# Kernel optimization log

Hardware: AMD Instinct MI355X
Metric: run time of the kernel (lower is better)

Reference implementation:

```python
import jax, jax.numpy as jnp
import numpy as np

EPS = 1e-05
NEG = -1e9

def rotate_half(x):
    x1, x2 = jnp.split(x, 2, axis=-1)
    return jnp.concatenate([-x2, x1], axis=-1)

def rmsnorm(x, w):
    xf = x.astype(jnp.float32)
    n = xf * jax.lax.rsqrt(jnp.mean(xf * xf, axis=-1, keepdims=True) + EPS)
    return w * n.astype(x.dtype)

def setup_inputs() -> dict:
    key = jax.random.key(0)
    ks = jax.random.split(key, 12)
    B, S, H, NH, DH, FF = 1, 2048, 2048, 16, 128, 8192
    x = jax.random.normal(ks[0], (B, S, H), jnp.float32)
    # additive causal mask [1,1,S,S]
    causal = jnp.where(jnp.tril(jnp.ones((S, S), bool)), 0.0, NEG).astype(jnp.float32)
    attention_mask = causal[None, None]
    alibi = 0.1 * jax.random.normal(ks[1], (1, NH, S, S), jnp.float32)
    # rotary angles [S, DH]
    inv = 1.0 / (10000.0 ** (jnp.arange(0, DH, 2, dtype=jnp.float32) / DH))
    ang = jnp.arange(S, dtype=jnp.float32)[:, None] * inv[None, :]
    freqs = jnp.concatenate([ang, ang], axis=-1)  # [S, DH]
    sc = 1.0 / np.sqrt(H)
    wq = sc * jax.random.normal(ks[2], (H, H), jnp.float32)
    wk = sc * jax.random.normal(ks[3], (H, H), jnp.float32)
    wv = sc * jax.random.normal(ks[4], (H, H), jnp.float32)
    wo = sc * jax.random.normal(ks[5], (H, H), jnp.float32)
    w1 = sc * jax.random.normal(ks[6], (H, FF), jnp.float32)
    w3 = sc * jax.random.normal(ks[7], (H, FF), jnp.float32)
    w2 = (1.0 / np.sqrt(FF)) * jax.random.normal(ks[8], (FF, H), jnp.float32)
    attn_norm_w = jnp.ones((H,), jnp.float32)
    ffn_norm_w = jnp.ones((H,), jnp.float32)
    return dict(x=x, attention_mask=attention_mask, alibi=alibi, freqs=freqs,
                wq=wq, wk=wk, wv=wv, wo=wo, w1=w1, w2=w2, w3=w3,
                attn_norm_w=attn_norm_w, ffn_norm_w=ffn_norm_w)

def reference(x, attention_mask, alibi, freqs, wq, wk, wv, wo, w1, w2, w3,
              attn_norm_w, ffn_norm_w):
    B, S, H = x.shape
    NH = 16
    DH = H // NH
    nx = rmsnorm(x, attn_norm_w)
    # projections -> [B, NH, S, DH]
    def heads(y):
        return y.reshape(B, S, NH, DH).transpose(0, 2, 1, 3)
    q = heads(nx @ wq)
    k = heads(nx @ wk)
    v = heads(nx @ wv)
    cos, sin = jnp.cos(freqs), jnp.sin(freqs)  # [S, DH] broadcasts over B,NH
    q = q * cos + rotate_half(q) * sin
    k = k * cos + rotate_half(k) * sin
    scores = jnp.einsum('bhqd,bhkd->bhqk', q, k) / np.sqrt(DH)
    scores = scores + attention_mask + alibi
    attn = jax.nn.softmax(scores, axis=-1)
    out = jnp.einsum('bhqk,bhkd->bhqd', attn, v)
    out = out.transpose(0, 2, 1, 3).reshape(B, S, H)
    x = x + out @ wo
    nx = rmsnorm(x, ffn_norm_w)
    ff = (jax.nn.silu(nx @ w1) * (nx @ w3)) @ w2
    return x + ff
```

## Files before the change

### kernel.cpp

```cpp
#include <hip/hip_runtime.h>
#include <hip/hip_bf16.h>
#include <math.h>

typedef __bf16 bf16x8 __attribute__((ext_vector_type(8)));
typedef float  f32x4  __attribute__((ext_vector_type(4)));
typedef unsigned short u16x8 __attribute__((ext_vector_type(8)));
typedef unsigned short u16x4 __attribute__((ext_vector_type(4)));

#define DEV static __device__ __forceinline__

DEV void gload16(const void* g, void* l) {
  __builtin_amdgcn_global_load_lds((__attribute__((address_space(1))) void*)g,
                                   (__attribute__((address_space(3))) void*)l,
                                   16, 0, 0);
}

DEV float bf2f(unsigned short u) {
  unsigned v = ((unsigned)u) << 16;
  return __builtin_bit_cast(float, v);
}
DEV unsigned short f2bf(float f) {
  unsigned u = __builtin_bit_cast(unsigned, f);
  u = u + 0x7fffu + ((u >> 16) & 1u);
  return (unsigned short)(u >> 16);
}

__global__ __launch_bounds__(256) void rmsnorm_k(const float* __restrict__ x,
    const float* __restrict__ w, unsigned short* __restrict__ out, int H) {
  int row = blockIdx.x;
  const float4* xr = (const float4*)(x + (size_t)row * H);
  float4 a = xr[threadIdx.x * 2], b = xr[threadIdx.x * 2 + 1];
  float ss = a.x*a.x + a.y*a.y + a.z*a.z + a.w*a.w
           + b.x*b.x + b.y*b.y + b.z*b.z + b.w*b.w;
#pragma unroll
  for (int o = 32; o; o >>= 1) ss += __shfl_down(ss, o, 64);
  __shared__ float red[4];
  if ((threadIdx.x & 63) == 0) red[threadIdx.x >> 6] = ss;
  __syncthreads();
  float rs = rsqrtf((red[0] + red[1] + red[2] + red[3]) * (1.0f / 2048.0f) + 1e-5f);
  size_t base = (size_t)row * H + threadIdx.x * 8;
  const float* wv = w + threadIdx.x * 8;
  float vals[8] = {a.x, a.y, a.z, a.w, b.x, b.y, b.z, b.w};
  u16x8 o8;
#pragma unroll
  for (int i = 0; i < 8; ++i) o8[i] = f2bf(vals[i] * rs * wv[i]);
  *(u16x8*)(out + base) = o8;
}

__global__ __launch_bounds__(256) void reduce4rms_k(const float* __restrict__ part,
    const float* __restrict__ resid, const float* __restrict__ w,
    float* __restrict__ x2, unsigned short* __restrict__ nxo, int H, size_t mn) {
  const int row = blockIdx.x, t = threadIdx.x;
  size_t base = (size_t)row * H + t * 8;
  float v[8];
  {
    float4 a = ((const float4*)(resid + base))[0];
    float4 b = ((const float4*)(resid + base))[1];
    v[0]=a.x; v[1]=a.y; v[2]=a.z; v[3]=a.w; v[4]=b.x; v[5]=b.y; v[6]=b.z; v[7]=b.w;
  }
#pragma unroll
  for (int s = 0; s < 4; ++s) {
    const float4* p4 = (const float4*)(part + (size_t)s * mn + base);
    float4 pa = p4[0], pb = p4[1];
    v[0]+=pa.x; v[1]+=pa.y; v[2]+=pa.z; v[3]+=pa.w;
    v[4]+=pb.x; v[5]+=pb.y; v[6]+=pb.z; v[7]+=pb.w;
  }
  float ss = 0.f;
#pragma unroll
  for (int i = 0; i < 8; ++i) ss += v[i] * v[i];
  float4 o0 = {v[0],v[1],v[2],v[3]}, o1 = {v[4],v[5],v[6],v[7]};
  ((float4*)(x2 + base))[0] = o0;
  ((float4*)(x2 + base))[1] = o1;
#pragma unroll
  for (int o = 32; o; o >>= 1) ss += __shfl_down(ss, o, 64);
  __shared__ float red[4];
  if ((t & 63) == 0) red[t >> 6] = ss;
  __syncthreads();
  float rs = rsqrtf((red[0] + red[1] + red[2] + red[3]) * (1.0f / 2048.0f) + 1e-5f);
  const float* wv = w + t * 8;
  u16x8 o8;
#pragma unroll
  for (int i = 0; i < 8; ++i) o8[i] = f2bf(v[i] * rs * wv[i]);
  *(u16x8*)(nxo + base) = o8;
}

DEV void wtrans_body(const float* __restrict__ W, unsigned short* __restrict__ Wt,
                     int R, int C, int ilv, int bx, int by, int t,
                     unsigned short (*tile)[68]) {
  const int c0 = bx * 64, r0 = by * 64;
  const int lr = t >> 4, lc4 = (t & 15) * 4;
#pragma unroll
  for (int i = 0; i < 4; ++i) {
    float4 v = *(const float4*)&W[(size_t)(r0 + lr + i * 16) * C + c0 + lc4];
    u16x4 s4;
    s4[0] = f2bf(v.x); s4[1] = f2bf(v.y); s4[2] = f2bf(v.z); s4[3] = f2bf(v.w);
    *(u16x4*)&tile[lr + i * 16][lc4] = s4;
  }
  __syncthreads();
  const int oc = t >> 3, seg = (t & 7) * 8;
#pragma unroll
  for (int i = 0; i < 2; ++i) {
    int c = c0 + oc + i * 32;
    u16x8 o8;
#pragma unroll
    for (int j = 0; j < 8; ++j) o8[j] = tile[seg + j][oc + i * 32];
    size_t dstrow = (ilv < 0) ? (size_t)c
                              : (size_t)(c >> 4) * 32 + (c & 15) + ilv * 16;
    *(u16x8*)&Wt[dstrow * R + r0 + seg] = o8;
  }
}

__global__ __launch_bounds__(256) void wtrans64_k(const float* __restrict__ W,
    unsigned short* __restrict__ Wt, int R, int C, int ilv) {
  __shared__ unsigned short tile[64][68];
  wtrans_body(W, Wt, R, C, ilv, blockIdx.x, blockIdx.y, threadIdx.x, tile);
}

__global__ __launch_bounds__(256) void wtrans4_k(
    const float* __restrict__ s0, const float* __restrict__ s1,
    const float* __restrict__ s2, const float* __restrict__ s3,
    unsigned short* __restrict__ d0, unsigned short* __restrict__ d1,
    unsigned short* __restrict__ d2, unsigned short* __restrict__ d3,
    int R, int C) {
  __shared__ unsigned short tile[64][68];
  const float* s = (blockIdx.z == 0) ? s0 : (blockIdx.z == 1) ? s1
                 : (blockIdx.z == 2) ? s2 : s3;
  unsigned short* d = (blockIdx.z == 0) ? d0 : (blockIdx.z == 1) ? d1
                    : (blockIdx.z == 2) ? d2 : d3;
  wtrans_body(s, d, R, C, -1, blockIdx.x, blockIdx.y, threadIdx.x, tile);
}

__global__ __launch_bounds__(256) void wtrans13_k(
    const float* __restrict__ w1, const float* __restrict__ w3,
    unsigned short* __restrict__ dst, int R, int C) {
  __shared__ unsigned short tile[64][68];
  const float* s = blockIdx.z ? w3 : w1;
  wtrans_body(s, dst, R, C, (int)blockIdx.z, blockIdx.x, blockIdx.y,
              threadIdx.x, tile);
}

#define STG_A(H, BUF, KC) do {                                                 \
    gload16(Asrc0 + (size_t)(H) * 128 * lda + (KC),                            \
            &lds[(BUF) * 16384 + (H) * 8192 + w * 1024]);                      \
    gload16(Asrc1 + (size_t)(H) * 128 * lda + (KC),                            \
            &lds[(BUF) * 16384 + (H) * 8192 + w * 1024 + 512]);                \
  } while (0)

#define STG_B(H, BUF, KC) do {                                                 \
    gload16(Bsrc0 + (size_t)(H) * 128 * ldb + (KC),                            \
            &lds[32768 + (BUF) * 16384 + (H) * 8192 + w * 1024]);              \
    gload16(Bsrc1 + (size_t)(H) * 128 * ldb + (KC),                            \
            &lds[32768 + (BUF) * 16384 + (H) * 8192 + w * 1024 + 512]);        \
  } while (0)

#define DS_A(DST, MH) do {                                                     \
    const int abase = buf * 16384 + (MH) * 8192 + arow * 64;                   \
    _Pragma("unroll") for (int m = 0; m < 4; ++m) {                            \
      DST[m][0] = *(const bf16x8*)&lds[abase + m * 1024 + acol0];              \
      DST[m][1] = *(const bf16x8*)&lds[abase + m * 1024 + acol1];              \
    } } while (0)

#define DS_B(DST, NH) do {                                                     \
    const int bbase = 32768 + buf * 16384 + (NH) * 8192 + brow * 64;           \
    _Pragma("unroll") for (int n = 0; n < 2; ++n) {                            \
      DST[n][0] = *(const bf16x8*)&lds[bbase + n * 1024 + acol0];              \
      DST[n][1] = *(const bf16x8*)&lds[bbase + n * 1024 + acol1];              \
    } } while (0)

#define MFMA16(AI, AR, BR) do {                                                \
    _Pragma("unroll") for (int m = 0; m < 4; ++m)                              \
      _Pragma("unroll") for (int n = 0; n < 2; ++n) {                          \
        acc[AI][m][n] = __builtin_amdgcn_mfma_f32_16x16x32_bf16(               \
            AR[m][0], BR[n][0], acc[AI][m][n], 0, 0, 0);                       \
        acc[AI][m][n] = __builtin_amdgcn_mfma_f32_16x16x32_bf16(               \
            AR[m][1], BR[n][1], acc[AI][m][n], 0, 0, 0);                       \
      }                                                                        \
  } while (0)

template <int EPI>
__global__ __launch_bounds__(512, 2) void gemm256_k(
    const unsigned short* __restrict__ A, int lda,
    const unsigned short* __restrict__ B, int ldb,
    unsigned short* __restrict__ Cb, float* __restrict__ Cf,
    int M, int N, int Kext) {
  __shared__ unsigned short lds[65536];
  const int t = threadIdx.x, w = t >> 6, lane = t & 63;
  const int nbm = M >> 8, nbn = N >> 8, nwg = nbm * nbn;
  int id = blockIdx.x;
  id = (id & 7) * (nwg >> 3) + (id >> 3);
  const int bm = id % nbm, bn = id / nbm;
  const size_t m0 = (size_t)bm << 8, n0 = (size_t)bn << 8;
  const int koff = blockIdx.y * Kext;
  const int NT = Kext >> 6;
  const int scol = ((lane & 7) ^ (lane >> 3)) * 8;
  const unsigned short* Asrc0 = A + (m0 + w * 16 + (lane >> 3)) * (size_t)lda + koff + scol;
  const unsigned short* Asrc1 = A + (m0 + w * 16 + 8 + (lane >> 3)) * (size_t)lda + koff + scol;
  const unsigned short* Bsrc0 = B + (n0 + w * 16 + (lane >> 3)) * (size_t)ldb + koff + scol;
  const unsigned short* Bsrc1 = B + (n0 + w * 16 + 8 + (lane >> 3)) * (size_t)ldb + koff + scol;
  const int arow = (w >> 2) * 64 + (lane & 15);
  const int brow = (w & 3) * 32 + (lane & 15);
  const int acol0 = ((lane >> 4) * 8) ^ ((lane & 7) << 3);
  const int acol1 = acol0 ^ 32;
  f32x4 acc[4][4][2] = {};
  bf16x8 Acur[4][2], B0r[2][2], B1r[2][2];
  STG_A(0, 0, 0); STG_B(0, 0, 0); STG_A(1, 0, 0); STG_B(1, 0, 0);
  STG_A(0, 1, 64); STG_B(0, 1, 64);
  asm volatile("s_waitcnt vmcnt(4)" ::: "memory");
  __builtin_amdgcn_s_barrier();
  for (int kt = 0; kt < NT; ++kt) {
    const int buf = kt & 1;
    const int kc1 = (kt + 1) * 64, kc2 = (kt + 2) * 64;
    const bool p1 = (kt + 1 < NT), p2 = (kt + 2 < NT);
    DS_A(Acur, 0); DS_B(B0r, 0); DS_B(B1r, 1);
    if (p1) { STG_A(1, buf ^ 1, kc1); STG_B(1, buf ^ 1, kc1); }
    __builtin_amdgcn_sched_barrier(0);
    __builtin_amdgcn_s_barrier();
    __builtin_amdgcn_s_setprio(1);
    MFMA16(0, Acur, B0r);
    MFMA16(1, Acur, B1r);
    __builtin_amdgcn_s_setprio(0);
    __builtin_amdgcn_sched_barrier(0);
    __builtin_amdgcn_s_barrier();
    DS_A(Acur, 1);
    if (p2) { STG_A(0, buf, kc2); STG_B(0, buf, kc2); }
    __builtin_amdgcn_sched_barrier(0);
    __builtin_amdgcn_s_barrier();
    __builtin_amdgcn_s_setprio(1);
    MFMA16(2, Acur, B0r);
    MFMA16(3, Acur, B1r);
    __builtin_amdgcn_s_setprio(0);
    __builtin_amdgcn_sched_barrier(0);
    if (p2) { asm volatile("s_waitcnt vmcnt(4)" ::: "memory"); }
    else    { asm volatile("s_waitcnt vmcnt(0)" ::: "memory"); }
    __builtin_amdgcn_s_barrier();
  }
#pragma unroll
  for (int Mh = 0; Mh < 2; ++Mh)
#pragma unroll
    for (int Nh = 0; Nh < 2; ++Nh)
#pragma unroll
      for (int m = 0; m < 4; ++m) {
        size_t gr = m0 + Mh * 128 + (w >> 2) * 64 + m * 16 + (lane >> 4) * 4;
        if constexpr (EPI == 2) {
          size_t gc = (n0 >> 1) + Nh * 64 + (w & 3) * 16 + (lane & 15);
          f32x4 v0 = acc[Mh * 2 + Nh][m][0];
          f32x4 v1 = acc[Mh * 2 + Nh][m][1];
#pragma unroll
          for (int j = 0; j < 4; ++j) {
            float s = v0[j] / (1.0f + __expf(-v0[j]));
            Cb[(gr + j) * (size_t)(N >> 1) + gc] = f2bf(s * v1[j]);
          }
        } else {
#pragma unroll
          for (int n = 0; n < 2; ++n) {
            size_t gc = n0 + Nh * 128 + (w & 3) * 32 + n * 16 + (lane & 15);
            f32x4 v = acc[Mh * 2 + Nh][m][n];
#pragma unroll
            for (int j = 0; j < 4; ++j) {
              size_t o = (gr + j) * (size_t)N + gc;
              if constexpr (EPI == 0) Cb[o] = f2bf(v[j]);
              else Cf[(size_t)blockIdx.y * M * N + o] = v[j];
            }
          }
        }
      }
}

__global__ __launch_bounds__(256) void rope_k(const unsigned short* __restrict__ qkv,
    const float* __restrict__ freqs, unsigned short* __restrict__ Qr,
    unsigned short* __restrict__ Kr, int S) {
  int idx = blockIdx.x * 256 + threadIdx.x;
  int dp = idx & 63, h = (idx >> 6) & 15, s = idx >> 10;
  float ang = freqs[s * 128 + dp];
  float c, sn;
  sincosf(ang, &sn, &c);
  size_t rq = (size_t)s * 6144 + h * 128 + dp;
  float q1 = bf2f(qkv[rq]),        q2 = bf2f(qkv[rq + 64]);
  float k1 = bf2f(qkv[rq + 2048]), k2 = bf2f(qkv[rq + 2048 + 64]);
  size_t ob = ((size_t)h * S + s) * 128 + dp;
  Qr[ob]      = f2bf(q1 * c - q2 * sn);
  Qr[ob + 64] = f2bf(q2 * c + q1 * sn);
  Kr[ob]      = f2bf(k1 * c - k2 * sn);
  Kr[ob + 64] = f2bf(k2 * c + k1 * sn);
}

__global__ __launch_bounds__(256) void vtrans_k(const unsigned short* __restrict__ qkv,
    unsigned short* __restrict__ Vt, int S) {
  __shared__ unsigned short tile[32][33];
  int h = blockIdx.z;
  int s0 = blockIdx.x * 32, d0 = blockIdx.y * 32;
  int tx = threadIdx.x, ty = threadIdx.y;
#pragma unroll
  for (int i = 0; i < 4; ++i)
    tile[ty + i * 8][tx] = qkv[(size_t)(s0 + ty + i * 8) * 6144 + 4096 + h * 128 + d0 + tx];
  __syncthreads();
#pragma unroll
  for (int i = 0; i < 4; ++i)
    Vt[((size_t)h * 128 + d0 + ty + i * 8) * S + s0 + tx] = tile[tx][ty + i * 8];
}

#define STGKV(KT, BUF) do {                                                    \
    _Pragma("unroll") for (int it = 0; it < 4; ++it)                           \
      gload16(Kb + (size_t)((KT) * 64 + it * 16 + sr) * 128 + scw,             \
              &lds[(BUF) * 8192 + (it * 16 + wave * 4) * 128]);                \
    _Pragma("unroll") for (int it = 0; it < 4; ++it)                           \
      gload16(Vb + (size_t)(it * 32 + vr) * S + (KT) * 64 + vcw,               \
              &lds[16384 + (BUF) * 8192 + (it * 32 + wave * 8) * 64]);         \
  } while (0)

#define ATTN_TILE(CUR, NXT, KT) do {                                           \
    const int buf = (KT) & 1;                                                  \
    const bool p1 = ((KT) + 1 < ktiles);                                       \
    if (p1) {                                                                  \
      STGKV((KT) + 1, buf ^ 1);                                                \
      _Pragma("unroll") for (int q8 = 0; q8 < 16; ++q8)                        \
        NXT[q8] = albase[(size_t)(q8 & 3) * S + ((KT) + 1) * 64 + (q8 >> 2) * 16]; \
      asm volatile("s_waitcnt vmcnt(24)" ::: "memory");                        \
    } else {                                                                   \
      asm volatile("s_waitcnt vmcnt(0)" ::: "memory");                         \
    }                                                                          \
    __builtin_amdgcn_s_barrier();                                              \
    f32x4 sf[4] = {};                                                          \
    _Pragma("unroll") for (int ks = 0; ks < 4; ++ks)                           \
      _Pragma("unroll") for (int n = 0; n < 4; ++n) {                          \
        bf16x8 kf = *(const bf16x8*)&lds[buf * 8192 + (n * 16 + row) * 128 +   \
                                         ((ks * 32 + kg) ^ kswz)];             \
        sf[n] = __builtin_amdgcn_mfma_f32_16x16x32_bf16(qf[ks], kf, sf[n], 0, 0, 0); \
      }                                                                        \
    float pv[4][4];                                                            \
    float tmax[4] = {-1e30f, -1e30f, -1e30f, -1e30f};                          \
    _Pragma("unroll") for (int n = 0; n < 4; ++n) {                            \
      int k_abs = (KT) * 64 + n * 16 + col;                                    \
      _Pragma("unroll") for (int j = 0; j < 4; ++j) {                          \
        int q_abs = q0 + wave * 16 + cg * 4 + j;                               \
        float v = sf[n][j] * scale + CUR[n * 4 + j];                           \
        if (k_abs > q_abs) v = -1e30f;                                         \
        pv[n][j] = v;                                                          \
        tmax[j] = fmaxf(tmax[j], v);                                           \
      } }                                                                      \
    _Pragma("unroll") for (int o2 = 1; o2 < 16; o2 <<= 1)                      \
      _Pragma("unroll") for (int j = 0; j < 4; ++j)                            \
        tmax[j] = fmaxf(tmax[j], __shfl_xor(tmax[j], o2, 64));                 \
    float alpha[4], rsum[4] = {};                                              \
    _Pragma("unroll") for (int j = 0; j < 4; ++j) {                            \
      float mn = fmaxf(m_run[j], tmax[j]);                                     \
      alpha[j] = __expf(m_run[j] - mn);                                        \
      m_run[j] = mn;                                                           \
    }                                                                          \
    _Pragma("unroll") for (int n = 0; n < 4; ++n)                              \
      _Pragma("unroll") for (int j = 0; j < 4; ++j) {                          \
        float p = __expf(pv[n][j] - m_run[j]);                                 \
        pv[n][j] = p;                                                          \
        rsum[j] += p;                                                          \
      }                                                                        \
    _Pragma("unroll") for (int o2 = 1; o2 < 16; o2 <<= 1)                      \
      _Pragma("unroll") for (int j = 0; j < 4; ++j)                            \
        rsum[j] += __shfl_xor(rsum[j], o2, 64);                                \
    _Pragma("unroll") for (int j = 0; j < 4; ++j)                              \
      l_run[j] = l_run[j] * alpha[j] + rsum[j];                                \
    _Pragma("unroll") for (int nn = 0; nn < 8; ++nn)                           \
      _Pragma("unroll") for (int j = 0; j < 4; ++j) o[nn][j] *= alpha[j];      \
    _Pragma("unroll") for (int n = 0; n < 4; ++n)                              \
      _Pragma("unroll") for (int j = 0; j < 4; ++j) {                          \
        int pr = cg * 4 + j;                                                   \
        pw[pr * 64 + ((n * 16 + col) ^ ((pr & 7) << 3))] = f2bf(pv[n][j]);     \
      }                                                                        \
    asm volatile("s_waitcnt lgkmcnt(0)" ::: "memory");                         \
    __builtin_amdgcn_sched_barrier(0);                                         \
    _Pragma("unroll") for (int kk = 0; kk < 2; ++kk) {                         \
      bf16x8 pf = *(const bf16x8*)&pw[row * 64 + ((kk * 32 + kg) ^ kswz)];     \
      _Pragma("unroll") for (int nn = 0; nn < 8; ++nn) {                       \
        bf16x8 vf = *(const bf16x8*)&lds[16384 + buf * 8192 +                  \
                                         (nn * 16 + row) * 64 +                \
                                         ((kk * 32 + kg) ^ kswz)];             \
        o[nn] = __builtin_amdgcn_mfma_f32_16x16x32_bf16(pf, vf, o[nn], 0, 0, 0); \
      } }                                                                      \
    __builtin_amdgcn_s_barrier();                                              \
  } while (0)

__global__ __launch_bounds__(256) void attn_k(
    const unsigned short* __restrict__ Qr, const unsigned short* __restrict__ Kr,
    const unsigned short* __restrict__ Vt, const float* __restrict__ alibi,
    unsigned short* __restrict__ Ao, int S) {
  __shared__ unsigned short lds[36864];
  const int t = threadIdx.x, wave = t >> 6, lane = t & 63;
  const int h = blockIdx.y, nq = gridDim.x, bx = blockIdx.x;
  const int qt = (bx & 1) ? (nq - 1 - (bx >> 1)) : (bx >> 1);
  const int q0 = qt * 64;
  const int sr = t >> 4, scw = ((t & 15) ^ ((t >> 4) & 7)) * 8;
  const int vr = t >> 3, vcw = ((t & 7) ^ ((t >> 3) & 7)) * 8;
  const unsigned short* Kb = Kr + (size_t)h * S * 128;
  const unsigned short* Vb = Vt + (size_t)h * 128 * S;
  const int row = lane & 15, kg = (lane >> 4) * 8, cg = lane >> 4, col = lane & 15;
  const int kswz = (lane & 7) << 3;
  bf16x8 qf[4];
  const unsigned short* Qrow = Qr + ((size_t)h * S + q0 + wave * 16 + row) * 128;
#pragma unroll
  for (int ks = 0; ks < 4; ++ks) qf[ks] = *(const bf16x8*)&Qrow[ks * 32 + kg];
  f32x4 o[8] = {};
  float m_run[4] = {-1e30f, -1e30f, -1e30f, -1e30f};
  float l_run[4] = {};
  unsigned short* pw = &lds[32768 + wave * 1024];
  const float scale = 0.08838834764831843f;
  const int ktiles = qt + 1;
  const float* albase = alibi + (size_t)h * S * S +
                        ((size_t)q0 + wave * 16 + cg * 4) * S + col;
  float alA[16], alB[16];
  STGKV(0, 0);
#pragma unroll
  for (int q8 = 0; q8 < 16; ++q8)
    alA[q8] = albase[(size_t)(q8 & 3) * S + (q8 >> 2) * 16];
  for (int kt = 0; kt < ktiles; kt += 2) {
    ATTN_TILE(alA, alB, kt);
    if (kt + 1 < ktiles) ATTN_TILE(alB, alA, kt + 1);
  }
#pragma unroll
  for (int nn = 0; nn < 8; ++nn)
#pragma unroll
    for (int j = 0; j < 4; ++j) {
      int q_abs = q0 + wave * 16 + cg * 4 + j;
      Ao[(size_t)q_abs * 2048 + h * 128 + nn * 16 + col] = f2bf(o[nn][j] / l_run[j]);
    }
}

__global__ __launch_bounds__(256) void reduce4_k(const float* __restrict__ part,
    const float* __restrict__ resid, float* __restrict__ out, int n4, size_t mn) {
  int i = blockIdx.x * 256 + threadIdx.x;
  if (i >= n4) return;
  const float4* p = (const float4*)part;
  size_t q = mn >> 2;
  float4 a = ((const float4*)resid)[i];
  float4 s0 = p[i], s1 = p[i + q], s2 = p[i + 2 * q], s3 = p[i + 3 * q];
  float4 r;
  r.x = a.x + s0.x + s1.x + s2.x + s3.x;
  r.y = a.y + s0.y + s1.y + s2.y + s3.y;
  r.z = a.z + s0.z + s1.z + s2.z + s3.z;
  r.w = a.w + s0.w + s1.w + s2.w + s3.w;
  ((float4*)out)[i] = r;
}

extern "C" void kernel_launch(void* const* d_in, const int* in_sizes, int n_in,
                              void* d_out, int out_size, void* d_ws, size_t ws_size,
                              hipStream_t stream) {
  const int S = 2048, H = 2048, NH = 16, DH = 128, FF = 8192;
  const float* x     = (const float*)d_in[0];
  const float* alibi = (const float*)d_in[2];
  const float* freqs = (const float*)d_in[3];
  const float* wq    = (const float*)d_in[4];
  const float* wk    = (const float*)d_in[5];
  const float* wv    = (const float*)d_in[6];
  const float* wo    = (const float*)d_in[7];
  const float* w1    = (const float*)d_in[8];
  const float* w2    = (const float*)d_in[9];
  const float* w3    = (const float*)d_in[10];
  const float* anw   = (const float*)d_in[11];
  const float* fnw   = (const float*)d_in[12];
  float* out = (float*)d_out;

  char* ws = (char*)d_ws;
  size_t off = 0;
  auto alloc = [&](size_t n) { char* p = ws + off; off += (n + 255) & ~(size_t)255; return p; };
  unsigned short* qkvT = (unsigned short*)alloc((size_t)3 * H * H * 2);
  unsigned short* woT  = (unsigned short*)alloc((size_t)H * H * 2);
  unsigned short* w13T = (unsigned short*)alloc((size_t)2 * FF * H * 2);
  unsigned short* w2T  = (unsigned short*)alloc((size_t)H * FF * 2);
  float*          x2   = (float*)alloc((size_t)S * H * 4);
  unsigned short* nx2  = (unsigned short*)alloc((size_t)S * H * 2);
  unsigned short* gbuf = (unsigned short*)alloc((size_t)S * FF * 2);
  unsigned short* nx   = (unsigned short*)alloc((size_t)S * H * 2);
  unsigned short* qkvb = (unsigned short*)alloc((size_t)S * 3 * H * 2);
  unsigned short* Qr   = (unsigned short*)alloc((size_t)NH * S * DH * 2);
  unsigned short* Kr   = (unsigned short*)alloc((size_t)NH * S * DH * 2);
  unsigned short* Vt   = (unsigned short*)alloc((size_t)NH * DH * S * 2);
  unsigned short* attno= (unsigned short*)alloc((size_t)S * H * 2);
  float* part4 = (float*)alloc((size_t)4 * S * H * 4);

  dim3 tb32(32, 8);
  wtrans4_k<<<dim3(32, 32, 4), 256, 0, stream>>>(
      wq, wk, wv, wo,
      qkvT, qkvT + (size_t)H * H, qkvT + (size_t)2 * H * H, woT, H, H);
  wtrans13_k<<<dim3(128, 32, 2), 256, 0, stream>>>(w1, w3, w13T, H, FF);
  wtrans64_k<<<dim3(32, 128), 256, 0, stream>>>(w2, w2T, FF, H, -1);

  rmsnorm_k<<<S, 256, 0, stream>>>(x, anw, nx, H);
  gemm256_k<0><<<dim3(192, 1), 512, 0, stream>>>(nx, H, qkvT, H, qkvb, nullptr, S, 3 * H, H);
  rope_k<<<(S * NH * 64) / 256, 256, 0, stream>>>(qkvb, freqs, Qr, Kr, S);
  vtrans_k<<<dim3(S / 32, DH / 32, NH), tb32, 0, stream>>>(qkvb, Vt, S);
  attn_k<<<dim3(S / 64, NH), 256, 0, stream>>>(Qr, Kr, Vt, alibi, attno, S);
  gemm256_k<1><<<dim3(64, 4), 512, 0, stream>>>(attno, H, woT, H, nullptr, part4, S, H, 512);
  reduce4rms_k<<<S, 256, 0, stream>>>(part4, x, fnw, x2, nx2, H, (size_t)S * H);
  gemm256_k<2><<<dim3(512, 1), 512, 0, stream>>>(nx2, H, w13T, H, gbuf, nullptr, S, 2 * FF, H);
  gemm256_k<1><<<dim3(64, 4), 512, 0, stream>>>(gbuf, FF, w2T, FF, nullptr, part4, S, H, FF / 4);
  reduce4_k<<<4096, 256, 0, stream>>>(part4, x2, out, S * H / 4, (size_t)S * H);
}
```

Before: 511.8 us.

## Fuse rope and V-transpose kernels; add lazy softmax rescale and MFMA priority

```diff
diff --git a/kernel.cpp b/kernel.cpp
--- a/kernel.cpp
+++ b/kernel.cpp
@@ -266,37 +266,37 @@
       }
 }
 
-__global__ __launch_bounds__(256) void rope_k(const unsigned short* __restrict__ qkv,
+__global__ __launch_bounds__(256) void ropevt_k(const unsigned short* __restrict__ qkv,
     const float* __restrict__ freqs, unsigned short* __restrict__ Qr,
-    unsigned short* __restrict__ Kr, int S) {
-  int idx = blockIdx.x * 256 + threadIdx.x;
-  int dp = idx & 63, h = (idx >> 6) & 15, s = idx >> 10;
-  float ang = freqs[s * 128 + dp];
-  float c, sn;
-  sincosf(ang, &sn, &c);
-  size_t rq = (size_t)s * 6144 + h * 128 + dp;
-  float q1 = bf2f(qkv[rq]),        q2 = bf2f(qkv[rq + 64]);
-  float k1 = bf2f(qkv[rq + 2048]), k2 = bf2f(qkv[rq + 2048 + 64]);
-  size_t ob = ((size_t)h * S + s) * 128 + dp;
-  Qr[ob]      = f2bf(q1 * c - q2 * sn);
-  Qr[ob + 64] = f2bf(q2 * c + q1 * sn);
-  Kr[ob]      = f2bf(k1 * c - k2 * sn);
-  Kr[ob + 64] = f2bf(k2 * c + k1 * sn);
-}
-
-__global__ __launch_bounds__(256) void vtrans_k(const unsigned short* __restrict__ qkv,
-    unsigned short* __restrict__ Vt, int S) {
-  __shared__ unsigned short tile[32][33];
-  int h = blockIdx.z;
-  int s0 = blockIdx.x * 32, d0 = blockIdx.y * 32;
-  int tx = threadIdx.x, ty = threadIdx.y;
-#pragma unroll
-  for (int i = 0; i < 4; ++i)
-    tile[ty + i * 8][tx] = qkv[(size_t)(s0 + ty + i * 8) * 6144 + 4096 + h * 128 + d0 + tx];
-  __syncthreads();
-#pragma unroll
-  for (int i = 0; i < 4; ++i)
-    Vt[((size_t)h * 128 + d0 + ty + i * 8) * S + s0 + tx] = tile[tx][ty + i * 8];
+    unsigned short* __restrict__ Kr, unsigned short* __restrict__ Vt, int S) {
+  if (blockIdx.x < 8192) {
+    int idx = blockIdx.x * 256 + threadIdx.x;
+    int dp = idx & 63, h = (idx >> 6) & 15, s = idx >> 10;
+    float ang = freqs[s * 128 + dp];
+    float c, sn;
+    sincosf(ang, &sn, &c);
+    size_t rq = (size_t)s * 6144 + h * 128 + dp;
+    float q1 = bf2f(qkv[rq]),        q2 = bf2f(qkv[rq + 64]);
+    float k1 = bf2f(qkv[rq + 2048]), k2 = bf2f(qkv[rq + 2048 + 64]);
+    size_t ob = ((size_t)h * S + s) * 128 + dp;
+    Qr[ob]      = f2bf(q1 * c - q2 * sn);
+    Qr[ob + 64] = f2bf(q2 * c + q1 * sn);
+    Kr[ob]      = f2bf(k1 * c - k2 * sn);
+    Kr[ob + 64] = f2bf(k2 * c + k1 * sn);
+  } else {
+    __shared__ unsigned short tile[32][33];
+    int vb = (int)blockIdx.x - 8192;
+    int h = vb >> 8, rem = vb & 255;
+    int s0 = (rem & 63) * 32, d0 = (rem >> 6) * 32;
+    int tx = threadIdx.x & 31, ty = threadIdx.x >> 5;
+#pragma unroll
+    for (int i = 0; i < 4; ++i)
+      tile[ty + i * 8][tx] = qkv[(size_t)(s0 + ty + i * 8) * 6144 + 4096 + h * 128 + d0 + tx];
+    __syncthreads();
+#pragma unroll
+    for (int i = 0; i < 4; ++i)
+      Vt[((size_t)h * 128 + d0 + ty + i * 8) * S + s0 + tx] = tile[tx][ty + i * 8];
+  }
 }
 
 #define STGKV(KT, BUF) do {                                                    \
@@ -321,45 +321,70 @@
     }                                                                          \
     __builtin_amdgcn_s_barrier();                                              \
     f32x4 sf[4] = {};                                                          \
+    __builtin_amdgcn_s_setprio(1);                                             \
     _Pragma("unroll") for (int ks = 0; ks < 4; ++ks)                           \
       _Pragma("unroll") for (int n = 0; n < 4; ++n) {                          \
         bf16x8 kf = *(const bf16x8*)&lds[buf * 8192 + (n * 16 + row) * 128 +   \
                                          ((ks * 32 + kg) ^ kswz)];             \
         sf[n] = __builtin_amdgcn_mfma_f32_16x16x32_bf16(qf[ks], kf, sf[n], 0, 0, 0); \
       }                                                                        \
+    __builtin_amdgcn_s_setprio(0);                                             \
     float pv[4][4];                                                            \
     float tmax[4] = {-1e30f, -1e30f, -1e30f, -1e30f};                          \
-    _Pragma("unroll") for (int n = 0; n < 4; ++n) {                            \
-      int k_abs = (KT) * 64 + n * 16 + col;                                    \
-      _Pragma("unroll") for (int j = 0; j < 4; ++j) {                          \
-        int q_abs = q0 + wave * 16 + cg * 4 + j;                               \
-        float v = sf[n][j] * scale + CUR[n * 4 + j];                           \
-        if (k_abs > q_abs) v = -1e30f;                                         \
-        pv[n][j] = v;                                                          \
-        tmax[j] = fmaxf(tmax[j], v);                                           \
-      } }                                                                      \
+    if ((KT) == ktiles - 1) {                                                  \
+      _Pragma("unroll") for (int n = 0; n < 4; ++n) {                          \
+        int k_abs = (KT) * 64 + n * 16 + col;                                  \
+        _Pragma("unroll") for (int j = 0; j < 4; ++j) {                        \
+          int q_abs = q0 + wave * 16 + cg * 4 + j;                             \
+          float v = sf[n][j] * scale + CUR[n * 4 + j];                         \
+          if (k_abs > q_abs) v = -1e30f;                                       \
+          pv[n][j] = v;                                                        \
+          tmax[j] = fmaxf(tmax[j], v);                                         \
+        } }                                                                    \
+    } else {                                                                   \
+      _Pragma("unroll") for (int n = 0; n < 4; ++n)                            \
+        _Pragma("unroll") for (int j = 0; j < 4; ++j) {                        \
+          float v = sf[n][j] * scale + CUR[n * 4 + j];                         \
+          pv[n][j] = v;                                                        \
+          tmax[j] = fmaxf(tmax[j], v);                                         \
+        }                                                                      \
+    }                                                                          \
     _Pragma("unroll") for (int o2 = 1; o2 < 16; o2 <<= 1)                      \
       _Pragma("unroll") for (int j = 0; j < 4; ++j)                            \
         tmax[j] = fmaxf(tmax[j], __shfl_xor(tmax[j], o2, 64));                 \
-    float alpha[4], rsum[4] = {};                                              \
-    _Pragma("unroll") for (int j = 0; j < 4; ++j) {                            \
-      float mn = fmaxf(m_run[j], tmax[j]);                                     \
-      alpha[j] = __expf(m_run[j] - mn);                                        \
-      m_run[j] = mn;                                                           \
+    float rsum[4] = {};                                                        \
+    float md = fmaxf(fmaxf(tmax[0] - m_run[0], tmax[1] - m_run[1]),            \
+                     fmaxf(tmax[2] - m_run[2], tmax[3] - m_run[3]));           \
+    if (__all(md <= 8.0f)) {                                                   \
+      _Pragma("unroll") for (int n = 0; n < 4; ++n)                            \
+        _Pragma("unroll") for (int j = 0; j < 4; ++j) {                        \
+          float p = __expf(pv[n][j] - m_run[j]);                               \
+          pv[n][j] = p;  rsum[j] += p;                                         \
+        }                                                                      \
+      _Pragma("unroll") for (int o2 = 1; o2 < 16; o2 <<= 1)                    \
+        _Pragma("unroll") for (int j = 0; j < 4; ++j)                          \
+          rsum[j] += __shfl_xor(rsum[j], o2, 64);                              \
+      _Pragma("unroll") for (int j = 0; j < 4; ++j) l_run[j] += rsum[j];       \
+    } else {                                                                   \
+      float alpha[4];                                                          \
+      _Pragma("unroll") for (int j = 0; j < 4; ++j) {                          \
+        float mn = fmaxf(m_run[j], tmax[j]);                                   \
+        alpha[j] = __expf(m_run[j] - mn);                                      \
+        m_run[j] = mn;                                                         \
+      }                                                                        \
+      _Pragma("unroll") for (int n = 0; n < 4; ++n)                            \
+        _Pragma("unroll") for (int j = 0; j < 4; ++j) {                        \
+          float p = __expf(pv[n][j] - m_run[j]);                               \
+          pv[n][j] = p;  rsum[j] += p;                                         \
+        }                                                                      \
+      _Pragma("unroll") for (int o2 = 1; o2 < 16; o2 <<= 1)                    \
+        _Pragma("unroll") for (int j = 0; j < 4; ++j)                          \
+          rsum[j] += __shfl_xor(rsum[j], o2, 64);                              \
+      _Pragma("unroll") for (int j = 0; j < 4; ++j)                            \
+        l_run[j] = l_run[j] * alpha[j] + rsum[j];                              \
+      _Pragma("unroll") for (int nn = 0; nn < 8; ++nn)                         \
+        _Pragma("unroll") for (int j = 0; j < 4; ++j) o[nn][j] *= alpha[j];    \
     }                                                                          \
-    _Pragma("unroll") for (int n = 0; n < 4; ++n)                              \
-      _Pragma("unroll") for (int j = 0; j < 4; ++j) {                          \
-        float p = __expf(pv[n][j] - m_run[j]);                                 \
-        pv[n][j] = p;                                                          \
-        rsum[j] += p;                                                          \
-      }                                                                        \
-    _Pragma("unroll") for (int o2 = 1; o2 < 16; o2 <<= 1)                      \
-      _Pragma("unroll") for (int j = 0; j < 4; ++j)                            \
-        rsum[j] += __shfl_xor(rsum[j], o2, 64);                                \
-    _Pragma("unroll") for (int j = 0; j < 4; ++j)                              \
-      l_run[j] = l_run[j] * alpha[j] + rsum[j];                                \
-    _Pragma("unroll") for (int nn = 0; nn < 8; ++nn)                           \
-      _Pragma("unroll") for (int j = 0; j < 4; ++j) o[nn][j] *= alpha[j];      \
     _Pragma("unroll") for (int n = 0; n < 4; ++n)                              \
       _Pragma("unroll") for (int j = 0; j < 4; ++j) {                          \
         int pr = cg * 4 + j;                                                   \
@@ -367,6 +392,7 @@
       }                                                                        \
     asm volatile("s_waitcnt lgkmcnt(0)" ::: "memory");                         \
     __builtin_amdgcn_sched_barrier(0);                                         \
+    __builtin_amdgcn_s_setprio(1);                                             \
     _Pragma("unroll") for (int kk = 0; kk < 2; ++kk) {                         \
       bf16x8 pf = *(const bf16x8*)&pw[row * 64 + ((kk * 32 + kg) ^ kswz)];     \
       _Pragma("unroll") for (int nn = 0; nn < 8; ++nn) {                       \
@@ -375,6 +401,7 @@
                                          ((kk * 32 + kg) ^ kswz)];             \
         o[nn] = __builtin_amdgcn_mfma_f32_16x16x32_bf16(pf, vf, o[nn], 0, 0, 0); \
       } }                                                                      \
+    __builtin_amdgcn_s_setprio(0);                                             \
     __builtin_amdgcn_s_barrier();                                              \
   } while (0)
 
@@ -475,7 +502,6 @@
   unsigned short* attno= (unsigned short*)alloc((size_t)S * H * 2);
   float* part4 = (float*)alloc((size_t)4 * S * H * 4);
 
-  dim3 tb32(32, 8);
   wtrans4_k<<<dim3(32, 32, 4), 256, 0, stream>>>(
       wq, wk, wv, wo,
       qkvT, qkvT + (size_t)H * H, qkvT + (size_t)2 * H * H, woT, H, H);
@@ -484,8 +510,7 @@
 
   rmsnorm_k<<<S, 256, 0, stream>>>(x, anw, nx, H);
   gemm256_k<0><<<dim3(192, 1), 512, 0, stream>>>(nx, H, qkvT, H, qkvb, nullptr, S, 3 * H, H);
-  rope_k<<<(S * NH * 64) / 256, 256, 0, stream>>>(qkvb, freqs, Qr, Kr, S);
-  vtrans_k<<<dim3(S / 32, DH / 32, NH), tb32, 0, stream>>>(qkvb, Vt, S);
+  ropevt_k<<<12288, 256, 0, stream>>>(qkvb, freqs, Qr, Kr, Vt, S);
   attn_k<<<dim3(S / 64, NH), 256, 0, stream>>>(Qr, Kr, Vt, alibi, attno, S);
   gemm256_k<1><<<dim3(64, 4), 512, 0, stream>>>(attno, H, woT, H, nullptr, part4, S, H, 512);
   reduce4rms_k<<<S, 256, 0, stream>>>(part4, x, fnw, x2, nx2, H, (size_t)S * H);
```

New measurement: 565.1 us. 10.4% more time.
